# Performance work log

Measured on AMD Instinct MI355X. Metric: run time of the kernel, lower is better.

The kernel has to match this reference:

```python
import jax, jax.numpy as jnp
import numpy as np

D_MODEL = 1024
NHEAD = 16
HEAD_DIM = D_MODEL // NHEAD
SCALE = 1.0 / np.sqrt(HEAD_DIM).astype(np.float32)
B, L = 2, 2048
NEG_INF = -1e30


def setup_inputs() -> dict:
    key = jax.random.key(0)
    ks = jax.random.split(key, 12)
    xav = np.sqrt(6.0 / (D_MODEL + D_MODEL)).astype(np.float32)  # xavier_uniform gain=1
    def lin_w(k):
        return jax.random.uniform(k, (D_MODEL, D_MODEL), jnp.float32, -xav, xav)
    x = jax.random.normal(ks[0], (B, L, D_MODEL), jnp.float32)
    role_mask = jax.random.randint(ks[1], (B, L), 0, 2, jnp.int32)
    # causal attention mask: True = masked (upper triangle above diagonal)
    attn_mask = jnp.triu(jnp.ones((L, L), jnp.bool_), k=1)
    # random key padding: True = padded key
    key_padding_mask = jax.random.randint(ks[2], (B, L), 0, 2, jnp.int32).astype(jnp.bool_)
    return {
        "x": x,
        "role_mask": role_mask,
        "attn_mask": attn_mask,
        "key_padding_mask": key_padding_mask,
        "Wq": lin_w(ks[3]), "bq": jnp.zeros((D_MODEL,), jnp.float32),
        "Wk": lin_w(ks[4]), "bk": jnp.zeros((D_MODEL,), jnp.float32),
        "Wv": lin_w(ks[5]), "bv": jnp.zeros((D_MODEL,), jnp.float32),
        "Wo": lin_w(ks[6]), "bo": jnp.zeros((D_MODEL,), jnp.float32),
        "delta": jnp.asarray(1.0, jnp.float32),
    }


def reference(x, role_mask, attn_mask, key_padding_mask,
              Wq, bq, Wk, bk, Wv, bv, Wo, bo, delta):
    Bb, Ll, Dd = x.shape
    def heads(t):  # [B,L,D] -> [B,H,L,hd]
        return t.reshape(Bb, Ll, NHEAD, HEAD_DIM).transpose(0, 2, 1, 3)
    Q = heads(x @ Wq.T + bq)
    K = heads(x @ Wk.T + bk)
    V = heads(x @ Wv.T + bv)
    scores = jnp.einsum('bhqd,bhkd->bhqk', Q, K) * SCALE  # [B,H,L,L]
    same_role = (role_mask[:, :, None] == role_mask[:, None, :])  # [B,L,L]
    scores = scores + (same_role.astype(scores.dtype) * delta)[:, None, :, :]
    scores = jnp.where(attn_mask[None, None, :, :], -jnp.inf, scores)
    scores = jnp.where(key_padding_mask[:, None, None, :], -jnp.inf, scores)
    attn = jax.nn.softmax(scores, axis=-1)
    attn = jnp.nan_to_num(attn, nan=0.0, posinf=0.0, neginf=0.0)
    out = jnp.einsum('bhqk,bhkd->bhqd', attn, V)
    out = out.transpose(0, 2, 1, 3).reshape(Bb, Ll, Dd)
    return out @ Wo.T + bo
```

## Files before the change

kernel.cpp:

```cpp
#include <hip/hip_runtime.h>
#include <hip/hip_bf16.h>

#define DM 1024
#define NH 16
#define HD 64
#define BB 2
#define LL 2048
#define BL (BB * LL)
#define SCALE 0.125f
#define NEG_BIG -1e30f
#define LOG2E 1.4426950408889634f
#define SC2 (SCALE * LOG2E)
#define FIXM 16.0f
#define SLOTB 8448
#define POOL0_SLOTS 960

typedef __bf16 bf16;
typedef __bf16 bf16x8 __attribute__((ext_vector_type(8)));
typedef __bf16 bf16x4 __attribute__((ext_vector_type(4)));
typedef float f32x4 __attribute__((ext_vector_type(4)));

static __device__ inline bf16x8 load8(const bf16* p) {
    return *reinterpret_cast<const bf16x8*>(p);
}

static __device__ inline float scrub(float x) {
    union { float f; unsigned u; } c; c.f = x;
    return ((c.u & 0x7F800000u) == 0x7F800000u) ? 0.f : x;
}

typedef __attribute__((address_space(1))) const unsigned char ga_t;
typedef __attribute__((address_space(3))) unsigned char ls_t;
static __device__ inline void gload_lds16(const void* g, void* l) {
    __builtin_amdgcn_global_load_lds((ga_t*)g, (ls_t*)l, 16, 0, 0);
}

__global__ __launch_bounds__(256) void prep_all(
    const float* __restrict__ x,
    const float* __restrict__ Wq, const float* __restrict__ Wk,
    const float* __restrict__ Wv, const float* __restrict__ Wo,
    bf16* __restrict__ xb, bf16* __restrict__ Wqb, bf16* __restrict__ Wkb,
    bf16* __restrict__ Wvb, bf16* __restrict__ Wob)
{
    const int tid = threadIdx.x;
    const int gid = blockIdx.x;
    const float* src; bf16* dst; size_t base;
    if (gid < 1024) { src = x; dst = xb; base = (size_t)gid * 1024; }
    else {
        const int wsel = (gid - 1024) >> 8;
        src = (wsel == 0) ? Wq : (wsel == 1) ? Wk : (wsel == 2) ? Wv : Wo;
        dst = (wsel == 0) ? Wqb : (wsel == 1) ? Wkb : (wsel == 2) ? Wvb : Wob;
        base = (size_t)((gid - 1024) & 255) * 1024;
    }
#pragma unroll
    for (int it = 0; it < 4; it++) {
        const size_t i = base + it * 256 + tid;
        const f32x4 v = ((const f32x4*)src)[i];
        bf16x4 o;
        o[0] = (bf16)v[0]; o[1] = (bf16)v[1]; o[2] = (bf16)v[2]; o[3] = (bf16)v[3];
        ((bf16x4*)dst)[i] = o;
    }
}

__global__ __launch_bounds__(256) void compact_meta(
    const int* __restrict__ role, const void* __restrict__ kpad,
    const float* __restrict__ deltap,
    float* __restrict__ biasC, int* __restrict__ cntq, int* __restrict__ cpos,
    bf16* __restrict__ kwc)
{
    const int b = blockIdx.x;
    const int tid = threadIdx.x;
    const unsigned char* kb = (const unsigned char*)kpad;
    int f3F = 0, fLow = 0, fOff = 0;
    for (int i = (tid & 63); i < BL; i += 64) {
        const unsigned char v = kb[i];
        if (v == 0x3F) f3F = 1;
        if ((i & 3) < 2 && v) fLow = 1;
        if ((i & 3) && v) fOff = 1;
    }
    const int mode = __any(f3F) ? (__any(fLow) ? 3 : 2) : (__any(fOff) ? 1 : 0);

    __shared__ int ssum[256];
    int loc[8]; int s = 0;
#pragma unroll
    for (int j = 0; j < 8; j++) {
        const int i = tid * 8 + j, idx = b * LL + i;
        const bool pad = (mode == 0) ? (((const int*)kpad)[idx] != 0)
                       : (mode == 1) ? (((const unsigned char*)kpad)[idx] != 0)
                       : (mode == 2) ? (((const float*)kpad)[idx] != 0.f)
                                     : (((const unsigned short*)kpad)[idx] != 0);
        loc[j] = pad ? 0 : 1; s += loc[j];
    }
    ssum[tid] = s; __syncthreads();
    for (int off = 1; off < 256; off <<= 1) {
        const int t = (tid >= off) ? ssum[tid - off] : 0;
        __syncthreads();
        ssum[tid] += t;
        __syncthreads();
    }
    const int nv = ssum[255];
    int run = ssum[tid] - s;
    const float d2 = scrub(deltap[0]) * LOG2E;
#pragma unroll
    for (int j = 0; j < 8; j++) {
        const int i = tid * 8 + j, idx = b * LL + i;
        const int inc = run + loc[j];
        cntq[idx] = inc;
        if (loc[j]) {
            const int cp = inc - 1;
            const int r = role[idx];
            biasC[b * LL + cp]      = -FIXM + ((r == 0) ? d2 : 0.f);
            biasC[BL + b * LL + cp] = -FIXM + ((r == 1) ? d2 : 0.f);
            cpos[idx] = cp;
        } else cpos[idx] = -1;
        run = inc;
    }
    for (int i = nv + tid; i < LL; i += 256) {
        biasC[b * LL + i] = NEG_BIG;
        biasC[BL + b * LL + i] = NEG_BIG;
    }
    const int roundv = (nv + 63) & ~63;
    const int nt = roundv - nv;
    bf16x8 z;
#pragma unroll
    for (int j = 0; j < 8; j++) z[j] = (bf16)0.f;
    for (int u = tid; u < nt * NH * 8; u += 256) {
        const int c8 = u & 7; const int t2 = u >> 3;
        const int h = t2 / nt; const int rr = nv + t2 % nt;
        *(bf16x8*)&kwc[(((size_t)(b * NH + h) * LL) + rr) * HD + c8 * 8] = z;
    }
}

__global__ __launch_bounds__(256) void qkv_bf16(
    const bf16* __restrict__ xb,
    const bf16* __restrict__ Wqb, const bf16* __restrict__ Wkb, const bf16* __restrict__ Wvb,
    const float* __restrict__ bq, const float* __restrict__ bk, const float* __restrict__ bv,
    bf16* __restrict__ qw, bf16* __restrict__ kwc, bf16* __restrict__ vwc,
    const int* __restrict__ cpos)
{
    __shared__ bf16 As[128 * 32];
    __shared__ bf16 Bs[128 * 32];
    const int tid = threadIdx.x;
    const int lane = tid & 63, w = tid >> 6;
    const int wm = w >> 1, wn = w & 1;
    const int ln = lane & 15, quad = lane >> 4;

    const int lin = blockIdx.y * 32 + blockIdx.x;
    const int xcd = lin & 7;
    const int t = lin >> 3;
    const int mloc = t & 3;
    const int yy = t >> 2;
    const int m0 = (xcd * 4 + mloc) * 128;
    const int sel = yy >> 3;
    const int nloc0 = (yy & 7) * 128;

    const bf16* Wb = (sel == 0) ? Wqb : ((sel == 1) ? Wkb : Wvb);
    const float* bias = (sel == 0) ? bq : ((sel == 1) ? bk : bv);
    bf16* dstw = (sel == 0) ? qw : ((sel == 1) ? kwc : vwc);

    const int rA = lane >> 2;
    const int cA = (lane & 3) * 8;

    f32x4 acc[4][4] = {};
    for (int k0 = 0; k0 < DM; k0 += 32) {
        __syncthreads();
#pragma unroll
        for (int s = 0; s < 2; s++) {
            const int r0 = s * 64 + w * 16;
            gload_lds16(xb + (size_t)(m0 + r0 + rA) * DM + k0 + cA, &As[r0 * 32]);
            gload_lds16(Wb + (size_t)(nloc0 + r0 + rA) * DM + k0 + cA, &Bs[r0 * 32]);
        }
        __syncthreads();
        bf16x8 a[4], b[4];
#pragma unroll
        for (int mi = 0; mi < 4; mi++)
            a[mi] = *(bf16x8*)&As[(wm * 64 + mi * 16 + ln) * 32 + quad * 8];
#pragma unroll
        for (int ni = 0; ni < 4; ni++)
            b[ni] = *(bf16x8*)&Bs[(wn * 64 + ni * 16 + ln) * 32 + quad * 8];
#pragma unroll
        for (int mi = 0; mi < 4; mi++)
#pragma unroll
            for (int ni = 0; ni < 4; ni++)
                acc[mi][ni] = __builtin_amdgcn_mfma_f32_16x16x32_bf16(a[mi], b[ni], acc[mi][ni], 0, 0, 0);
    }

#pragma unroll
    for (int mi = 0; mi < 4; mi++) {
#pragma unroll
        for (int i = 0; i < 4; i++) {
            const int row = m0 + wm * 64 + mi * 16 + quad * 4 + i;
            const int bb = row >> 11, llr = row & (LL - 1);
            const int cp = (sel == 0) ? llr : cpos[bb * LL + llr];
#pragma unroll
            for (int ni = 0; ni < 4; ni++) {
                const int ncol = nloc0 + wn * 64 + ni * 16 + ln;
                const int hh = ncol >> 6, dd = ncol & 63;
                const bf16 v = (bf16)scrub(acc[mi][ni][i] + bias[ncol]);
                if (cp >= 0)
                    dstw[(((size_t)(bb * NH + hh) * LL) + cp) * HD + dd] = v;
            }
        }
    }
}

__global__ __launch_bounds__(256) void vtrans(
    const bf16* __restrict__ vwc, bf16* __restrict__ vtc, const int* __restrict__ cntq)
{
    __shared__ bf16 T[64][72];
    const int l0 = blockIdx.x * 64;
    const int bh = blockIdx.y;
    const int b = bh >> 4;
    const int nv = cntq[b * LL + LL - 1];
    if (l0 >= ((nv + 63) & ~63)) return;
    const int tid = threadIdx.x;
#pragma unroll
    for (int it = 0; it < 2; it++) {
        const int idx = it * 256 + tid;
        const int row = idx >> 3, c8 = (idx & 7) * 8;
        const int wc = (((c8 >> 3) ^ ((row >> 3) & 7))) * 8;
        bf16x8 val;
#pragma unroll
        for (int j = 0; j < 8; j++) val[j] = (bf16)0.f;
        if (l0 + row < nv) val = load8(vwc + ((size_t)bh * LL + l0 + row) * HD + c8);
        *(bf16x8*)&T[row][wc] = val;
    }
    __syncthreads();
#pragma unroll
    for (int it = 0; it < 2; it++) {
        const int idx = it * 256 + tid;
        const int dd = idx >> 3, pg = (idx & 7) * 8;
        bf16x8 o;
#pragma unroll
        for (int j = 0; j < 8; j++) {
            const int r = pg + j;
            o[j] = T[r][(dd & 7) + ((((dd >> 3) ^ ((r >> 3) & 7))) << 3)];
        }
        *(bf16x8*)(vtc + ((size_t)bh * HD + dd) * LL + l0 + pg) = o;
    }
}

__global__ __launch_bounds__(256) void attn_v14(
    const bf16* __restrict__ qw, const bf16* __restrict__ kwc, const bf16* __restrict__ vtc,
    const int* __restrict__ role, const float* __restrict__ biasC, const int* __restrict__ cntq,
    char* __restrict__ pool0, char* __restrict__ pool1,
    bf16* __restrict__ attn_out)
{
    const int lin = blockIdx.y * 60 + blockIdx.x;
    const int xcd = lin & 7;
    const int t = lin >> 3;
    const int xg = t % 60;
    const int g = t / 60;
    const int bh = g * 8 + xcd;

    int qb, c;
    if (xg < 24)      { qb = 31 - xg / 3; c = xg % 3; }
    else if (xg < 48) { qb = 23 - (xg - 24) / 2; c = (xg - 24) % 2; }
    else              { qb = 59 - xg; c = 0; }
    const int nch = (qb + 12) / 12;

    __shared__ bf16 Ks[2][2][64 * 32];
    __shared__ bf16 Vs[2][2][64 * 32];

    const int tid = threadIdx.x;
    const int lane = tid & 63, w = tid >> 6;
    const int col = lane & 15, quad = lane >> 4;
    const int h = bh & (NH - 1), b = bh >> 4;
    const int q0 = qb * 64 + w * 16;

    const bf16* qbase = qw + (size_t)((b * NH + h) * LL) * HD;
    const bf16* kbase = kwc + (size_t)((b * NH + h) * LL) * HD;
    const bf16* vbase = vtc + (size_t)((b * NH + h) * HD) * LL;
    const int* rrow = role + b * LL;

    const int srow = lane >> 2;
    const int sslot = w * 16 + srow;
    const int trueK = ((sslot >> 5) & 1) * 32 + ((sslot >> 2) & 3) * 8
                    + ((sslot >> 4) & 1) * 4 + (sslot & 3);
    const int swz = ((lane & 3) ^ ((lane >> 3) & 3)) * 8;
    const bf16* ksrc = kbase + (size_t)trueK * HD + swz;
    const bf16* vsrc = vbase + (size_t)(w * 16 + srow) * LL + swz;

    bf16x8 qf[2];
    qf[0] = load8(qbase + (size_t)(q0 + col) * HD + quad * 8);
    qf[1] = load8(qbase + (size_t)(q0 + col) * HD + 32 + quad * 8);

    bf16x8 ones;
#pragma unroll
    for (int j = 0; j < 8; j++) ones[j] = (bf16)1.0f;

    const int qabs = q0 + col;
    const int role_q = rrow[qabs];
    const int cnt_q = cntq[b * LL + qabs];
    const float* bp = biasC + (size_t)role_q * BL + b * LL;

    const int cb = cntq[b * LL + qb * 64 + 63];
    const int Tb = (cb + 63) >> 6;
    const int t0c = (c * Tb) / nch;
    const int t1c = ((c + 1) * Tb) / nch;

    f32x4 ol = {};
    f32x4 o[4] = {};

    if (t0c < t1c) {
        const int kp = t0c * 64;
#pragma unroll
        for (int st = 0; st < 2; st++)
            gload_lds16(ksrc + (size_t)kp * HD + st * 32, &Ks[0][st][w * 512]);
#pragma unroll
        for (int kh = 0; kh < 2; kh++)
            gload_lds16(vsrc + kp + kh * 32, &Vs[0][kh][w * 512]);
    }

    const int rs = (quad ^ ((col >> 1) & 3)) * 8;

    for (int kt = t0c; kt < t1c; kt++) {
        const int cur = (kt - t0c) & 1;
        __syncthreads();

        if (kt + 1 < t1c) {
            const int k1 = (kt + 1) * 64;
#pragma unroll
            for (int st = 0; st < 2; st++)
                gload_lds16(ksrc + (size_t)k1 * HD + st * 32, &Ks[cur ^ 1][st][w * 512]);
#pragma unroll
            for (int kh = 0; kh < 2; kh++)
                gload_lds16(vsrc + k1 + kh * 32, &Vs[cur ^ 1][kh][w * 512]);
        }

        const int k0 = kt * 64;

        f32x4 s[4] = {};
#pragma unroll
        for (int st = 0; st < 2; st++) {
#pragma unroll
            for (int ns = 0; ns < 4; ns++) {
                const bf16x8 kf = *(bf16x8*)&Ks[cur][st][(ns * 16 + col) * 32 + rs];
                s[ns] = __builtin_amdgcn_mfma_f32_16x16x32_bf16(kf, qf[st], s[ns], 0, 0, 0);
            }
        }

        bf16x8 pf[2];
#pragma unroll
        for (int ns = 0; ns < 4; ns++) {
            const int kb_ = k0 + ((ns >> 1) << 5) + (quad << 3) + ((ns & 1) << 2);
            const f32x4 bv4 = *(const f32x4*)&bp[kb_];
#pragma unroll
            for (int i = 0; i < 4; i++) {
                float sv = fmaf(s[ns][i], SC2, bv4[i]);
                if ((kb_ + i) >= cnt_q) sv = NEG_BIG;
                pf[ns >> 1][(ns & 1) * 4 + i] = (bf16)exp2f(sv);
            }
        }

#pragma unroll
        for (int ns = 0; ns < 4; ns++) {
#pragma unroll
            for (int kh = 0; kh < 2; kh++) {
                const bf16x8 vf = *(bf16x8*)&Vs[cur][kh][(ns * 16 + col) * 32 + rs];
                o[ns] = __builtin_amdgcn_mfma_f32_16x16x32_bf16(vf, pf[kh], o[ns], 0, 0, 0);
            }
        }
#pragma unroll
        for (int kh = 0; kh < 2; kh++)
            ol = __builtin_amdgcn_mfma_f32_16x16x32_bf16(ones, pf[kh], ol, 0, 0, 0);
    }

    if (nch == 1) {
        const float inv = (ol[0] > 0.f) ? 1.f / ol[0] : 0.f;
        bf16* orow = attn_out + ((size_t)(b * LL) + qabs) * DM + h * HD;
#pragma unroll
        for (int ns = 0; ns < 4; ns++) {
            bf16x4 ov;
#pragma unroll
            for (int i = 0; i < 4; i++) ov[i] = (bf16)scrub(o[ns][i] * inv);
            *(bf16x4*)&orow[ns * 16 + quad * 4] = ov;
        }
    } else {
        const int base = (qb <= 23) ? (qb - 12) * 2 : 24 + (qb - 24) * 3;
        const int slot = bh * 48 + base + c;
        char* ptr = (slot < POOL0_SLOTS) ? (pool0 + (size_t)slot * SLOTB)
                                         : (pool1 + (size_t)(slot - POOL0_SLOTS) * SLOTB);
        bf16* op = (bf16*)ptr;
        float* lp = (float*)(ptr + 8192);
        const int r = w * 16 + col;
        if (quad == 0) lp[r] = ol[0];
#pragma unroll
        for (int ns = 0; ns < 4; ns++) {
            bf16x4 ov;
#pragma unroll
            for (int i = 0; i < 4; i++) ov[i] = (bf16)scrub(o[ns][i]);
            *(bf16x4*)&op[r * 64 + ns * 16 + quad * 4] = ov;
        }
    }
}

__global__ __launch_bounds__(256) void combine(
    const char* __restrict__ pool0, const char* __restrict__ pool1,
    bf16* __restrict__ attn_out)
{
    const int qb = 12 + blockIdx.x;
    const int bh = blockIdx.y;
    const int h = bh & (NH - 1), b = bh >> 4;
    const int nch = (qb + 12) / 12;
    const int base = (qb <= 23) ? (qb - 12) * 2 : 24 + (qb - 24) * 3;

    const char* ptr[3];
    for (int c = 0; c < nch; c++) {
        const int slot = bh * 48 + base + c;
        ptr[c] = (slot < POOL0_SLOTS) ? (pool0 + (size_t)slot * SLOTB)
                                      : (pool1 + (size_t)(slot - POOL0_SLOTS) * SLOTB);
    }

    __shared__ float linv[64];
    const int tid = threadIdx.x;
    if (tid < 64) {
        float ls = 0.f;
        for (int c = 0; c < nch; c++) ls += ((const float*)(ptr[c] + 8192))[tid];
        linv[tid] = (ls > 0.f) ? 1.f / ls : 0.f;
    }
    __syncthreads();

    const int r = tid >> 2;
    const int d0 = (tid & 3) * 16;
    float acc[16] = {};
    for (int c = 0; c < nch; c++) {
        const bf16* op = (const bf16*)ptr[c];
#pragma unroll
        for (int half = 0; half < 2; half++) {
            const bf16x8 v = load8(op + r * 64 + d0 + half * 8);
#pragma unroll
            for (int j = 0; j < 8; j++) acc[half * 8 + j] += (float)v[j];
        }
    }
    const float inv = linv[r];
    bf16x8 outv[2];
#pragma unroll
    for (int half = 0; half < 2; half++)
#pragma unroll
        for (int j = 0; j < 8; j++)
            outv[half][j] = (bf16)scrub(acc[half * 8 + j] * inv);
    bf16* orow = attn_out + ((size_t)(b * LL) + qb * 64 + r) * DM + h * HD + d0;
    *(bf16x8*)orow = outv[0];
    *(bf16x8*)(orow + 8) = outv[1];
}

__global__ __launch_bounds__(256) void out_bf16(
    const bf16* __restrict__ A, const bf16* __restrict__ Wb,
    const float* __restrict__ bias, float* __restrict__ out)
{
    __shared__ bf16 As[128 * 32];
    __shared__ bf16 Bs[64 * 32];
    const int tid = threadIdx.x;
    const int lane = tid & 63, w = tid >> 6;
    const int ln = lane & 15, quad = lane >> 4;

    const int lin = blockIdx.y * 32 + blockIdx.x;
    const int xcd = lin & 7;
    const int t = lin >> 3;
    const int mloc = t & 3;
    const int n = t >> 2;
    const int m0 = (xcd * 4 + mloc) * 128;
    const int n0 = n * 64;

    const int rA = lane >> 2;
    const int cA = (lane & 3) * 8;

    f32x4 acc[2][4] = {};
    for (int k0 = 0; k0 < DM; k0 += 32) {
        __syncthreads();
#pragma unroll
        for (int s = 0; s < 2; s++) {
            const int r0 = s * 64 + w * 16;
            gload_lds16(A + (size_t)(m0 + r0 + rA) * DM + k0 + cA, &As[r0 * 32]);
        }
        gload_lds16(Wb + (size_t)(n0 + w * 16 + rA) * DM + k0 + cA, &Bs[w * 16 * 32]);
        __syncthreads();
        bf16x8 a[2], b[4];
#pragma unroll
        for (int mi = 0; mi < 2; mi++)
            a[mi] = *(bf16x8*)&As[(w * 32 + mi * 16 + ln) * 32 + quad * 8];
#pragma unroll
        for (int ni = 0; ni < 4; ni++)
            b[ni] = *(bf16x8*)&Bs[(ni * 16 + ln) * 32 + quad * 8];
#pragma unroll
        for (int mi = 0; mi < 2; mi++)
#pragma unroll
            for (int ni = 0; ni < 4; ni++)
                acc[mi][ni] = __builtin_amdgcn_mfma_f32_16x16x32_bf16(a[mi], b[ni], acc[mi][ni], 0, 0, 0);
    }
#pragma unroll
    for (int mi = 0; mi < 2; mi++) {
#pragma unroll
        for (int ni = 0; ni < 4; ni++) {
            const int ncol = n0 + ni * 16 + ln;
            const float bv_ = bias[ncol];
#pragma unroll
            for (int i = 0; i < 4; i++) {
                const int row = m0 + w * 32 + mi * 16 + quad * 4 + i;
                out[(size_t)row * DM + ncol] = scrub(acc[mi][ni][i] + bv_);
            }
        }
    }
}

extern "C" void kernel_launch(void* const* d_in, const int* in_sizes, int n_in,
                              void* d_out, int out_size, void* d_ws, size_t ws_size,
                              hipStream_t stream) {
    const float* x    = (const float*)d_in[0];
    const int*   role = (const int*)d_in[1];
    const void*  kpad = d_in[3];
    const float* Wq = (const float*)d_in[4];
    const float* bq = (const float*)d_in[5];
    const float* Wk = (const float*)d_in[6];
    const float* bk = (const float*)d_in[7];
    const float* Wv = (const float*)d_in[8];
    const float* bv = (const float*)d_in[9];
    const float* Wo = (const float*)d_in[10];
    const float* bo = (const float*)d_in[11];
    const float* dl = (const float*)d_in[12];

    char* ws = (char*)d_ws;
    bf16* qw   = (bf16*)(ws);
    bf16* kwc  = (bf16*)(ws + (size_t)(8u  << 20));
    bf16* Wqb  = (bf16*)(ws + (size_t)(16u << 20));
    bf16* Wkb  = (bf16*)(ws + (size_t)(18u << 20));
    bf16* Wvb  = (bf16*)(ws + (size_t)(20u << 20));
    char* pool0 = ws + (size_t)(16u << 20);
    bf16* vwc  = (bf16*)(ws + (size_t)(24u << 20));
    bf16* aw   = (bf16*)(ws + (size_t)(24u << 20));
    bf16* vtc  = (bf16*)(ws + (size_t)(32u << 20));
    bf16* xb   = (bf16*)(ws + (size_t)(40u << 20));
    char* pool1 = ws + (size_t)(40u << 20);
    float* biasC = (float*)(ws + (size_t)(48u << 20));
    int*   cntq  = (int*)(ws + (size_t)(48u << 20) + 32768);
    int*   cpos  = (int*)(ws + (size_t)(48u << 20) + 49152);
    bf16* Wob  = (bf16*)(ws + (size_t)(48u << 20) + 65536);
    float* out = (float*)d_out;

    prep_all<<<dim3(2048), dim3(256), 0, stream>>>(
        x, Wq, Wk, Wv, Wo, xb, Wqb, Wkb, Wvb, Wob);
    compact_meta<<<dim3(2), dim3(256), 0, stream>>>(
        role, kpad, dl, biasC, cntq, cpos, kwc);
    qkv_bf16<<<dim3(32, 24), dim3(256), 0, stream>>>(
        xb, Wqb, Wkb, Wvb, bq, bk, bv, qw, kwc, vwc, cpos);
    vtrans<<<dim3(32, 32), dim3(256), 0, stream>>>(vwc, vtc, cntq);
    attn_v14<<<dim3(60, 32), dim3(256), 0, stream>>>(
        qw, kwc, vtc, role, biasC, cntq, pool0, pool1, aw);
    combine<<<dim3(20, 32), dim3(256), 0, stream>>>(pool0, pool1, aw);
    out_bf16<<<dim3(32, 16), dim3(256), 0, stream>>>(aw, Wob, bo, out);
}
```

Baseline: 218.4 us.

## Fuse meta compaction into prep kernel and widen GEMM K-tiles with XOR swizzle

Merges the compact_meta kernel into prep_all as two extra blocks, removing one kernel launch. The QKV and output-projection GEMMs now stage K-tiles of 64 instead of 32, with XOR-swizzled LDS columns to avoid bank conflicts. This halves the number of barrier pairs per GEMM. The cost is double the LDS footprint per block, which may lower occupancy.

```diff
diff --git a/kernel.cpp b/kernel.cpp
--- a/kernel.cpp
+++ b/kernel.cpp
@@ -40,36 +40,34 @@
     const float* __restrict__ Wq, const float* __restrict__ Wk,
     const float* __restrict__ Wv, const float* __restrict__ Wo,
     bf16* __restrict__ xb, bf16* __restrict__ Wqb, bf16* __restrict__ Wkb,
-    bf16* __restrict__ Wvb, bf16* __restrict__ Wob)
-{
-    const int tid = threadIdx.x;
-    const int gid = blockIdx.x;
-    const float* src; bf16* dst; size_t base;
-    if (gid < 1024) { src = x; dst = xb; base = (size_t)gid * 1024; }
-    else {
-        const int wsel = (gid - 1024) >> 8;
-        src = (wsel == 0) ? Wq : (wsel == 1) ? Wk : (wsel == 2) ? Wv : Wo;
-        dst = (wsel == 0) ? Wqb : (wsel == 1) ? Wkb : (wsel == 2) ? Wvb : Wob;
-        base = (size_t)((gid - 1024) & 255) * 1024;
-    }
-#pragma unroll
-    for (int it = 0; it < 4; it++) {
-        const size_t i = base + it * 256 + tid;
-        const f32x4 v = ((const f32x4*)src)[i];
-        bf16x4 o;
-        o[0] = (bf16)v[0]; o[1] = (bf16)v[1]; o[2] = (bf16)v[2]; o[3] = (bf16)v[3];
-        ((bf16x4*)dst)[i] = o;
-    }
-}
-
-__global__ __launch_bounds__(256) void compact_meta(
+    bf16* __restrict__ Wvb, bf16* __restrict__ Wob,
     const int* __restrict__ role, const void* __restrict__ kpad,
     const float* __restrict__ deltap,
     float* __restrict__ biasC, int* __restrict__ cntq, int* __restrict__ cpos,
     bf16* __restrict__ kwc)
 {
-    const int b = blockIdx.x;
     const int tid = threadIdx.x;
+    const int gid = blockIdx.x;
+    if (gid < 2048) {
+        const float* src; bf16* dst; size_t base;
+        if (gid < 1024) { src = x; dst = xb; base = (size_t)gid * 1024; }
+        else {
+            const int wsel = (gid - 1024) >> 8;
+            src = (wsel == 0) ? Wq : (wsel == 1) ? Wk : (wsel == 2) ? Wv : Wo;
+            dst = (wsel == 0) ? Wqb : (wsel == 1) ? Wkb : (wsel == 2) ? Wvb : Wob;
+            base = (size_t)((gid - 1024) & 255) * 1024;
+        }
+#pragma unroll
+        for (int it = 0; it < 4; it++) {
+            const size_t i = base + it * 256 + tid;
+            const f32x4 v = ((const f32x4*)src)[i];
+            bf16x4 o;
+            o[0] = (bf16)v[0]; o[1] = (bf16)v[1]; o[2] = (bf16)v[2]; o[3] = (bf16)v[3];
+            ((bf16x4*)dst)[i] = o;
+        }
+        return;
+    }
+    const int b = gid - 2048;
     const unsigned char* kb = (const unsigned char*)kpad;
     int f3F = 0, fLow = 0, fOff = 0;
     for (int i = (tid & 63); i < BL; i += 64) {
@@ -138,8 +136,8 @@
     bf16* __restrict__ qw, bf16* __restrict__ kwc, bf16* __restrict__ vwc,
     const int* __restrict__ cpos)
 {
-    __shared__ bf16 As[128 * 32];
-    __shared__ bf16 Bs[128 * 32];
+    __shared__ bf16 As[128 * 64];
+    __shared__ bf16 Bs[128 * 64];
     const int tid = threadIdx.x;
     const int lane = tid & 63, w = tid >> 6;
     const int wm = w >> 1, wn = w & 1;
@@ -158,31 +156,36 @@
     const float* bias = (sel == 0) ? bq : ((sel == 1) ? bk : bv);
     bf16* dstw = (sel == 0) ? qw : ((sel == 1) ? kwc : vwc);
 
-    const int rA = lane >> 2;
-    const int cA = (lane & 3) * 8;
+    const int r8 = lane >> 3;
+    const int swzc = ((lane & 7) ^ r8) * 8;
+    const int lsw = ln & 7;
 
     f32x4 acc[4][4] = {};
-    for (int k0 = 0; k0 < DM; k0 += 32) {
-        __syncthreads();
-#pragma unroll
-        for (int s = 0; s < 2; s++) {
-            const int r0 = s * 64 + w * 16;
-            gload_lds16(xb + (size_t)(m0 + r0 + rA) * DM + k0 + cA, &As[r0 * 32]);
-            gload_lds16(Wb + (size_t)(nloc0 + r0 + rA) * DM + k0 + cA, &Bs[r0 * 32]);
-        }
-        __syncthreads();
-        bf16x8 a[4], b[4];
-#pragma unroll
-        for (int mi = 0; mi < 4; mi++)
-            a[mi] = *(bf16x8*)&As[(wm * 64 + mi * 16 + ln) * 32 + quad * 8];
-#pragma unroll
-        for (int ni = 0; ni < 4; ni++)
-            b[ni] = *(bf16x8*)&Bs[(wn * 64 + ni * 16 + ln) * 32 + quad * 8];
-#pragma unroll
-        for (int mi = 0; mi < 4; mi++)
+    for (int k0 = 0; k0 < DM; k0 += 64) {
+        __syncthreads();
+#pragma unroll
+        for (int s = 0; s < 4; s++) {
+            const int r0 = s * 32 + w * 8;
+            gload_lds16(xb + (size_t)(m0 + r0 + r8) * DM + k0 + swzc, &As[r0 * 64]);
+            gload_lds16(Wb + (size_t)(nloc0 + r0 + r8) * DM + k0 + swzc, &Bs[r0 * 64]);
+        }
+        __syncthreads();
+#pragma unroll
+        for (int kk = 0; kk < 2; kk++) {
+            const int rc = ((kk * 4 + quad) ^ lsw) * 8;
+            bf16x8 a[4], b[4];
+#pragma unroll
+            for (int mi = 0; mi < 4; mi++)
+                a[mi] = *(bf16x8*)&As[(wm * 64 + mi * 16 + ln) * 64 + rc];
 #pragma unroll
             for (int ni = 0; ni < 4; ni++)
-                acc[mi][ni] = __builtin_amdgcn_mfma_f32_16x16x32_bf16(a[mi], b[ni], acc[mi][ni], 0, 0, 0);
+                b[ni] = *(bf16x8*)&Bs[(wn * 64 + ni * 16 + ln) * 64 + rc];
+#pragma unroll
+            for (int mi = 0; mi < 4; mi++)
+#pragma unroll
+                for (int ni = 0; ni < 4; ni++)
+                    acc[mi][ni] = __builtin_amdgcn_mfma_f32_16x16x32_bf16(a[mi], b[ni], acc[mi][ni], 0, 0, 0);
+        }
     }
 
 #pragma unroll
@@ -449,8 +452,8 @@
     const bf16* __restrict__ A, const bf16* __restrict__ Wb,
     const float* __restrict__ bias, float* __restrict__ out)
 {
-    __shared__ bf16 As[128 * 32];
-    __shared__ bf16 Bs[64 * 32];
+    __shared__ bf16 As[128 * 64];
+    __shared__ bf16 Bs[64 * 64];
     const int tid = threadIdx.x;
     const int lane = tid & 63, w = tid >> 6;
     const int ln = lane & 15, quad = lane >> 4;
@@ -463,31 +466,40 @@
     const int m0 = (xcd * 4 + mloc) * 128;
     const int n0 = n * 64;
 
-    const int rA = lane >> 2;
-    const int cA = (lane & 3) * 8;
+    const int r8 = lane >> 3;
+    const int swzc = ((lane & 7) ^ r8) * 8;
+    const int lsw = ln & 7;
 
     f32x4 acc[2][4] = {};
-    for (int k0 = 0; k0 < DM; k0 += 32) {
-        __syncthreads();
+    for (int k0 = 0; k0 < DM; k0 += 64) {
+        __syncthreads();
+#pragma unroll
+        for (int s = 0; s < 4; s++) {
+            const int r0 = s * 32 + w * 8;
+            gload_lds16(A + (size_t)(m0 + r0 + r8) * DM + k0 + swzc, &As[r0 * 64]);
+        }
 #pragma unroll
         for (int s = 0; s < 2; s++) {
-            const int r0 = s * 64 + w * 16;
-            gload_lds16(A + (size_t)(m0 + r0 + rA) * DM + k0 + cA, &As[r0 * 32]);
-        }
-        gload_lds16(Wb + (size_t)(n0 + w * 16 + rA) * DM + k0 + cA, &Bs[w * 16 * 32]);
-        __syncthreads();
-        bf16x8 a[2], b[4];
-#pragma unroll
-        for (int mi = 0; mi < 2; mi++)
-            a[mi] = *(bf16x8*)&As[(w * 32 + mi * 16 + ln) * 32 + quad * 8];
-#pragma unroll
-        for (int ni = 0; ni < 4; ni++)
-            b[ni] = *(bf16x8*)&Bs[(ni * 16 + ln) * 32 + quad * 8];
-#pragma unroll
-        for (int mi = 0; mi < 2; mi++)
+            const int r0 = s * 32 + w * 8;
+            gload_lds16(Wb + (size_t)(n0 + r0 + r8) * DM + k0 + swzc, &Bs[r0 * 64]);
+        }
+        __syncthreads();
+#pragma unroll
+        for (int kk = 0; kk < 2; kk++) {
+            const int rc = ((kk * 4 + quad) ^ lsw) * 8;
+            bf16x8 a[2], b[4];
+#pragma unroll
+            for (int mi = 0; mi < 2; mi++)
+                a[mi] = *(bf16x8*)&As[(w * 32 + mi * 16 + ln) * 64 + rc];
 #pragma unroll
             for (int ni = 0; ni < 4; ni++)
-                acc[mi][ni] = __builtin_amdgcn_mfma_f32_16x16x32_bf16(a[mi], b[ni], acc[mi][ni], 0, 0, 0);
+                b[ni] = *(bf16x8*)&Bs[(ni * 16 + ln) * 64 + rc];
+#pragma unroll
+            for (int mi = 0; mi < 2; mi++)
+#pragma unroll
+                for (int ni = 0; ni < 4; ni++)
+                    acc[mi][ni] = __builtin_amdgcn_mfma_f32_16x16x32_bf16(a[mi], b[ni], acc[mi][ni], 0, 0, 0);
+        }
     }
 #pragma unroll
     for (int mi = 0; mi < 2; mi++) {
@@ -538,9 +550,8 @@
     bf16* Wob  = (bf16*)(ws + (size_t)(48u << 20) + 65536);
     float* out = (float*)d_out;
 
-    prep_all<<<dim3(2048), dim3(256), 0, stream>>>(
-        x, Wq, Wk, Wv, Wo, xb, Wqb, Wkb, Wvb, Wob);
-    compact_meta<<<dim3(2), dim3(256), 0, stream>>>(
+    prep_all<<<dim3(2050), dim3(256), 0, stream>>>(
+        x, Wq, Wk, Wv, Wo, xb, Wqb, Wkb, Wvb, Wob,
         role, kpad, dl, biasC, cntq, cpos, kwc);
     qkv_bf16<<<dim3(32, 24), dim3(256), 0, stream>>>(
         xb, Wqb, Wkb, Wvb, bq, bk, bv, qw, kwc, vwc, cpos);
```

Result: slower. 224.9 us (+3.0%).

## Double-buffer LDS in projection GEMMs and merge metadata prep into conversion kernel

Applied to the files above, without the earlier changes.

The QKV and output projection GEMMs now use two LDS buffers. The next K-tile's global-to-LDS loads are issued before the current tile's MFMAs, which halves the barriers per iteration and overlaps memory latency with compute. The small compact_meta kernel is folded into prep_all as two extra blocks, removing a kernel launch. LDS usage doubles per block, which may reduce occupancy.

```diff
diff --git a/kernel.cpp b/kernel.cpp
--- a/kernel.cpp
+++ b/kernel.cpp
@@ -40,36 +40,34 @@
     const float* __restrict__ Wq, const float* __restrict__ Wk,
     const float* __restrict__ Wv, const float* __restrict__ Wo,
     bf16* __restrict__ xb, bf16* __restrict__ Wqb, bf16* __restrict__ Wkb,
-    bf16* __restrict__ Wvb, bf16* __restrict__ Wob)
-{
-    const int tid = threadIdx.x;
-    const int gid = blockIdx.x;
-    const float* src; bf16* dst; size_t base;
-    if (gid < 1024) { src = x; dst = xb; base = (size_t)gid * 1024; }
-    else {
-        const int wsel = (gid - 1024) >> 8;
-        src = (wsel == 0) ? Wq : (wsel == 1) ? Wk : (wsel == 2) ? Wv : Wo;
-        dst = (wsel == 0) ? Wqb : (wsel == 1) ? Wkb : (wsel == 2) ? Wvb : Wob;
-        base = (size_t)((gid - 1024) & 255) * 1024;
-    }
-#pragma unroll
-    for (int it = 0; it < 4; it++) {
-        const size_t i = base + it * 256 + tid;
-        const f32x4 v = ((const f32x4*)src)[i];
-        bf16x4 o;
-        o[0] = (bf16)v[0]; o[1] = (bf16)v[1]; o[2] = (bf16)v[2]; o[3] = (bf16)v[3];
-        ((bf16x4*)dst)[i] = o;
-    }
-}
-
-__global__ __launch_bounds__(256) void compact_meta(
+    bf16* __restrict__ Wvb, bf16* __restrict__ Wob,
     const int* __restrict__ role, const void* __restrict__ kpad,
     const float* __restrict__ deltap,
     float* __restrict__ biasC, int* __restrict__ cntq, int* __restrict__ cpos,
     bf16* __restrict__ kwc)
 {
-    const int b = blockIdx.x;
     const int tid = threadIdx.x;
+    const int gid = blockIdx.x;
+    if (gid < 2048) {
+        const float* src; bf16* dst; size_t base;
+        if (gid < 1024) { src = x; dst = xb; base = (size_t)gid * 1024; }
+        else {
+            const int wsel = (gid - 1024) >> 8;
+            src = (wsel == 0) ? Wq : (wsel == 1) ? Wk : (wsel == 2) ? Wv : Wo;
+            dst = (wsel == 0) ? Wqb : (wsel == 1) ? Wkb : (wsel == 2) ? Wvb : Wob;
+            base = (size_t)((gid - 1024) & 255) * 1024;
+        }
+#pragma unroll
+        for (int it = 0; it < 4; it++) {
+            const size_t i = base + it * 256 + tid;
+            const f32x4 v = ((const f32x4*)src)[i];
+            bf16x4 o;
+            o[0] = (bf16)v[0]; o[1] = (bf16)v[1]; o[2] = (bf16)v[2]; o[3] = (bf16)v[3];
+            ((bf16x4*)dst)[i] = o;
+        }
+        return;
+    }
+    const int b = gid - 2048;
     const unsigned char* kb = (const unsigned char*)kpad;
     int f3F = 0, fLow = 0, fOff = 0;
     for (int i = (tid & 63); i < BL; i += 64) {
@@ -138,8 +136,8 @@
     bf16* __restrict__ qw, bf16* __restrict__ kwc, bf16* __restrict__ vwc,
     const int* __restrict__ cpos)
 {
-    __shared__ bf16 As[128 * 32];
-    __shared__ bf16 Bs[128 * 32];
+    __shared__ bf16 As[2][128 * 32];
+    __shared__ bf16 Bs[2][128 * 32];
     const int tid = threadIdx.x;
     const int lane = tid & 63, w = tid >> 6;
     const int wm = w >> 1, wn = w & 1;
@@ -160,29 +158,42 @@
 
     const int rA = lane >> 2;
     const int cA = (lane & 3) * 8;
+    const bf16* asrc = xb + (size_t)(m0 + rA) * DM + cA;
+    const bf16* bsrc = Wb + (size_t)(nloc0 + rA) * DM + cA;
+
+#pragma unroll
+    for (int s = 0; s < 2; s++) {
+        const int r0 = s * 64 + w * 16;
+        gload_lds16(asrc + (size_t)r0 * DM, &As[0][r0 * 32]);
+        gload_lds16(bsrc + (size_t)r0 * DM, &Bs[0][r0 * 32]);
+    }
+    __syncthreads();
 
     f32x4 acc[4][4] = {};
+    int cur = 0;
     for (int k0 = 0; k0 < DM; k0 += 32) {
-        __syncthreads();
-#pragma unroll
-        for (int s = 0; s < 2; s++) {
-            const int r0 = s * 64 + w * 16;
-            gload_lds16(xb + (size_t)(m0 + r0 + rA) * DM + k0 + cA, &As[r0 * 32]);
-            gload_lds16(Wb + (size_t)(nloc0 + r0 + rA) * DM + k0 + cA, &Bs[r0 * 32]);
-        }
-        __syncthreads();
+        if (k0 + 32 < DM) {
+#pragma unroll
+            for (int s = 0; s < 2; s++) {
+                const int r0 = s * 64 + w * 16;
+                gload_lds16(asrc + (size_t)r0 * DM + k0 + 32, &As[cur ^ 1][r0 * 32]);
+                gload_lds16(bsrc + (size_t)r0 * DM + k0 + 32, &Bs[cur ^ 1][r0 * 32]);
+            }
+        }
         bf16x8 a[4], b[4];
 #pragma unroll
         for (int mi = 0; mi < 4; mi++)
-            a[mi] = *(bf16x8*)&As[(wm * 64 + mi * 16 + ln) * 32 + quad * 8];
+            a[mi] = *(bf16x8*)&As[cur][(wm * 64 + mi * 16 + ln) * 32 + quad * 8];
 #pragma unroll
         for (int ni = 0; ni < 4; ni++)
-            b[ni] = *(bf16x8*)&Bs[(wn * 64 + ni * 16 + ln) * 32 + quad * 8];
+            b[ni] = *(bf16x8*)&Bs[cur][(wn * 64 + ni * 16 + ln) * 32 + quad * 8];
 #pragma unroll
         for (int mi = 0; mi < 4; mi++)
 #pragma unroll
             for (int ni = 0; ni < 4; ni++)
                 acc[mi][ni] = __builtin_amdgcn_mfma_f32_16x16x32_bf16(a[mi], b[ni], acc[mi][ni], 0, 0, 0);
+        __syncthreads();
+        cur ^= 1;
     }
 
 #pragma unroll
@@ -449,8 +460,8 @@
     const bf16* __restrict__ A, const bf16* __restrict__ Wb,
     const float* __restrict__ bias, float* __restrict__ out)
 {
-    __shared__ bf16 As[128 * 32];
-    __shared__ bf16 Bs[64 * 32];
+    __shared__ bf16 As[2][128 * 32];
+    __shared__ bf16 Bs[2][64 * 32];
     const int tid = threadIdx.x;
     const int lane = tid & 63, w = tid >> 6;
     const int ln = lane & 15, quad = lane >> 4;
@@ -465,29 +476,42 @@
 
     const int rA = lane >> 2;
     const int cA = (lane & 3) * 8;
+    const bf16* asrc = A + (size_t)(m0 + rA) * DM + cA;
+    const bf16* bsrc = Wb + (size_t)(n0 + rA) * DM + cA;
+
+#pragma unroll
+    for (int s = 0; s < 2; s++) {
+        const int r0 = s * 64 + w * 16;
+        gload_lds16(asrc + (size_t)r0 * DM, &As[0][r0 * 32]);
+    }
+    gload_lds16(bsrc + (size_t)(w * 16) * DM, &Bs[0][w * 16 * 32]);
+    __syncthreads();
 
     f32x4 acc[2][4] = {};
+    int cur = 0;
     for (int k0 = 0; k0 < DM; k0 += 32) {
-        __syncthreads();
-#pragma unroll
-        for (int s = 0; s < 2; s++) {
-            const int r0 = s * 64 + w * 16;
-            gload_lds16(A + (size_t)(m0 + r0 + rA) * DM + k0 + cA, &As[r0 * 32]);
-        }
-        gload_lds16(Wb + (size_t)(n0 + w * 16 + rA) * DM + k0 + cA, &Bs[w * 16 * 32]);
-        __syncthreads();
+        if (k0 + 32 < DM) {
+#pragma unroll
+            for (int s = 0; s < 2; s++) {
+                const int r0 = s * 64 + w * 16;
+                gload_lds16(asrc + (size_t)r0 * DM + k0 + 32, &As[cur ^ 1][r0 * 32]);
+            }
+            gload_lds16(bsrc + (size_t)(w * 16) * DM + k0 + 32, &Bs[cur ^ 1][w * 16 * 32]);
+        }
         bf16x8 a[2], b[4];
 #pragma unroll
         for (int mi = 0; mi < 2; mi++)
-            a[mi] = *(bf16x8*)&As[(w * 32 + mi * 16 + ln) * 32 + quad * 8];
+            a[mi] = *(bf16x8*)&As[cur][(w * 32 + mi * 16 + ln) * 32 + quad * 8];
 #pragma unroll
         for (int ni = 0; ni < 4; ni++)
-            b[ni] = *(bf16x8*)&Bs[(ni * 16 + ln) * 32 + quad * 8];
+            b[ni] = *(bf16x8*)&Bs[cur][(ni * 16 + ln) * 32 + quad * 8];
 #pragma unroll
         for (int mi = 0; mi < 2; mi++)
 #pragma unroll
             for (int ni = 0; ni < 4; ni++)
                 acc[mi][ni] = __builtin_amdgcn_mfma_f32_16x16x32_bf16(a[mi], b[ni], acc[mi][ni], 0, 0, 0);
+        __syncthreads();
+        cur ^= 1;
     }
 #pragma unroll
     for (int mi = 0; mi < 2; mi++) {
@@ -538,9 +562,8 @@
     bf16* Wob  = (bf16*)(ws + (size_t)(48u << 20) + 65536);
     float* out = (float*)d_out;
 
-    prep_all<<<dim3(2048), dim3(256), 0, stream>>>(
-        x, Wq, Wk, Wv, Wo, xb, Wqb, Wkb, Wvb, Wob);
-    compact_meta<<<dim3(2), dim3(256), 0, stream>>>(
+    prep_all<<<dim3(2050), dim3(256), 0, stream>>>(
+        x, Wq, Wk, Wv, Wo, xb, Wqb, Wkb, Wvb, Wob,
         role, kpad, dl, biasC, cntq, cpos, kwc);
     qkv_bf16<<<dim3(32, 24), dim3(256), 0, stream>>>(
         xb, Wqb, Wkb, Wvb, bq, bk, bv, qw, kwc, vwc, cpos);
```

New measurement: 223.8 us. 1.02x slower.

## Fuse metadata compaction into prep kernel and gather-compact K/V projection rows

Applied to the files above, without the earlier changes.

Merges the compact_meta kernel into prep_all as two extra blocks, removing one kernel launch. The metadata pass now writes an inverse index (compact position to source row) instead of a forward scatter index. The K/V projection blocks gather only the non-padded input rows through that index and exit early for tiles beyond the valid count, so roughly half of the K/V GEMM work (padded keys) is skipped. Risks: the gathered A-tile loads are less contiguous, and correctness depends on the padding count being read before the tiles run.

```diff
diff --git a/kernel.cpp b/kernel.cpp
--- a/kernel.cpp
+++ b/kernel.cpp
@@ -40,36 +40,34 @@
     const float* __restrict__ Wq, const float* __restrict__ Wk,
     const float* __restrict__ Wv, const float* __restrict__ Wo,
     bf16* __restrict__ xb, bf16* __restrict__ Wqb, bf16* __restrict__ Wkb,
-    bf16* __restrict__ Wvb, bf16* __restrict__ Wob)
+    bf16* __restrict__ Wvb, bf16* __restrict__ Wob,
+    const int* __restrict__ role, const void* __restrict__ kpad,
+    const float* __restrict__ deltap,
+    float* __restrict__ biasC, int* __restrict__ cntq, int* __restrict__ ipos,
+    bf16* __restrict__ kwc)
 {
     const int tid = threadIdx.x;
     const int gid = blockIdx.x;
-    const float* src; bf16* dst; size_t base;
-    if (gid < 1024) { src = x; dst = xb; base = (size_t)gid * 1024; }
-    else {
-        const int wsel = (gid - 1024) >> 8;
-        src = (wsel == 0) ? Wq : (wsel == 1) ? Wk : (wsel == 2) ? Wv : Wo;
-        dst = (wsel == 0) ? Wqb : (wsel == 1) ? Wkb : (wsel == 2) ? Wvb : Wob;
-        base = (size_t)((gid - 1024) & 255) * 1024;
-    }
-#pragma unroll
-    for (int it = 0; it < 4; it++) {
-        const size_t i = base + it * 256 + tid;
-        const f32x4 v = ((const f32x4*)src)[i];
-        bf16x4 o;
-        o[0] = (bf16)v[0]; o[1] = (bf16)v[1]; o[2] = (bf16)v[2]; o[3] = (bf16)v[3];
-        ((bf16x4*)dst)[i] = o;
-    }
-}
-
-__global__ __launch_bounds__(256) void compact_meta(
-    const int* __restrict__ role, const void* __restrict__ kpad,
-    const float* __restrict__ deltap,
-    float* __restrict__ biasC, int* __restrict__ cntq, int* __restrict__ cpos,
-    bf16* __restrict__ kwc)
-{
-    const int b = blockIdx.x;
-    const int tid = threadIdx.x;
+    if (gid < 2048) {
+        const float* src; bf16* dst; size_t base;
+        if (gid < 1024) { src = x; dst = xb; base = (size_t)gid * 1024; }
+        else {
+            const int wsel = (gid - 1024) >> 8;
+            src = (wsel == 0) ? Wq : (wsel == 1) ? Wk : (wsel == 2) ? Wv : Wo;
+            dst = (wsel == 0) ? Wqb : (wsel == 1) ? Wkb : (wsel == 2) ? Wvb : Wob;
+            base = (size_t)((gid - 1024) & 255) * 1024;
+        }
+#pragma unroll
+        for (int it = 0; it < 4; it++) {
+            const size_t i = base + it * 256 + tid;
+            const f32x4 v = ((const f32x4*)src)[i];
+            bf16x4 o;
+            o[0] = (bf16)v[0]; o[1] = (bf16)v[1]; o[2] = (bf16)v[2]; o[3] = (bf16)v[3];
+            ((bf16x4*)dst)[i] = o;
+        }
+        return;
+    }
+    const int b = gid - 2048;
     const unsigned char* kb = (const unsigned char*)kpad;
     int f3F = 0, fLow = 0, fOff = 0;
     for (int i = (tid & 63); i < BL; i += 64) {
@@ -111,8 +109,8 @@
             const int r = role[idx];
             biasC[b * LL + cp]      = -FIXM + ((r == 0) ? d2 : 0.f);
             biasC[BL + b * LL + cp] = -FIXM + ((r == 1) ? d2 : 0.f);
-            cpos[idx] = cp;
-        } else cpos[idx] = -1;
+            ipos[b * LL + cp] = i;
+        }
         run = inc;
     }
     for (int i = nv + tid; i < LL; i += 256) {
@@ -136,7 +134,7 @@
     const bf16* __restrict__ Wqb, const bf16* __restrict__ Wkb, const bf16* __restrict__ Wvb,
     const float* __restrict__ bq, const float* __restrict__ bk, const float* __restrict__ bv,
     bf16* __restrict__ qw, bf16* __restrict__ kwc, bf16* __restrict__ vwc,
-    const int* __restrict__ cpos)
+    const int* __restrict__ ipos, const int* __restrict__ cntq)
 {
     __shared__ bf16 As[128 * 32];
     __shared__ bf16 Bs[128 * 32];
@@ -150,9 +148,19 @@
     const int t = lin >> 3;
     const int mloc = t & 3;
     const int yy = t >> 2;
-    const int m0 = (xcd * 4 + mloc) * 128;
+    const int mt = xcd * 4 + mloc;
     const int sel = yy >> 3;
     const int nloc0 = (yy & 7) * 128;
+
+    int b = 0, cp0 = 0, nvb = 0, m0 = 0;
+    if (sel == 0) {
+        m0 = mt * 128;
+    } else {
+        b = mt >> 4;
+        cp0 = (mt & 15) * 128;
+        nvb = cntq[b * LL + LL - 1];
+        if (cp0 >= nvb) return;
+    }
 
     const bf16* Wb = (sel == 0) ? Wqb : ((sel == 1) ? Wkb : Wvb);
     const float* bias = (sel == 0) ? bq : ((sel == 1) ? bk : bv);
@@ -161,44 +169,63 @@
     const int rA = lane >> 2;
     const int cA = (lane & 3) * 8;
 
+    const bf16* asrc[2];
+#pragma unroll
+    for (int s = 0; s < 2; s++) {
+        const int r = s * 64 + w * 16 + rA;
+        int grow;
+        if (sel == 0) grow = m0 + r;
+        else {
+            const int cp = cp0 + r;
+            grow = b * LL + ((cp < nvb) ? ipos[b * LL + cp] : 0);
+        }
+        asrc[s] = xb + (size_t)grow * DM + cA;
+    }
+
     f32x4 acc[4][4] = {};
     for (int k0 = 0; k0 < DM; k0 += 32) {
         __syncthreads();
 #pragma unroll
         for (int s = 0; s < 2; s++) {
             const int r0 = s * 64 + w * 16;
-            gload_lds16(xb + (size_t)(m0 + r0 + rA) * DM + k0 + cA, &As[r0 * 32]);
+            gload_lds16(asrc[s] + k0, &As[r0 * 32]);
             gload_lds16(Wb + (size_t)(nloc0 + r0 + rA) * DM + k0 + cA, &Bs[r0 * 32]);
         }
         __syncthreads();
-        bf16x8 a[4], b[4];
+        bf16x8 a[4], bfr[4];
 #pragma unroll
         for (int mi = 0; mi < 4; mi++)
             a[mi] = *(bf16x8*)&As[(wm * 64 + mi * 16 + ln) * 32 + quad * 8];
 #pragma unroll
         for (int ni = 0; ni < 4; ni++)
-            b[ni] = *(bf16x8*)&Bs[(wn * 64 + ni * 16 + ln) * 32 + quad * 8];
+            bfr[ni] = *(bf16x8*)&Bs[(wn * 64 + ni * 16 + ln) * 32 + quad * 8];
 #pragma unroll
         for (int mi = 0; mi < 4; mi++)
 #pragma unroll
             for (int ni = 0; ni < 4; ni++)
-                acc[mi][ni] = __builtin_amdgcn_mfma_f32_16x16x32_bf16(a[mi], b[ni], acc[mi][ni], 0, 0, 0);
+                acc[mi][ni] = __builtin_amdgcn_mfma_f32_16x16x32_bf16(a[mi], bfr[ni], acc[mi][ni], 0, 0, 0);
     }
 
 #pragma unroll
     for (int mi = 0; mi < 4; mi++) {
 #pragma unroll
         for (int i = 0; i < 4; i++) {
-            const int row = m0 + wm * 64 + mi * 16 + quad * 4 + i;
-            const int bb = row >> 11, llr = row & (LL - 1);
-            const int cp = (sel == 0) ? llr : cpos[bb * LL + llr];
+            const int rr = wm * 64 + mi * 16 + quad * 4 + i;
+            int batch, drow; bool valid;
+            if (sel == 0) {
+                const int row = m0 + rr;
+                batch = row >> 11; drow = row & (LL - 1); valid = true;
+            } else {
+                const int cp = cp0 + rr;
+                batch = b; drow = cp; valid = (cp < nvb);
+            }
 #pragma unroll
             for (int ni = 0; ni < 4; ni++) {
                 const int ncol = nloc0 + wn * 64 + ni * 16 + ln;
                 const int hh = ncol >> 6, dd = ncol & 63;
                 const bf16 v = (bf16)scrub(acc[mi][ni][i] + bias[ncol]);
-                if (cp >= 0)
-                    dstw[(((size_t)(bb * NH + hh) * LL) + cp) * HD + dd] = v;
+                if (valid)
+                    dstw[(((size_t)(batch * NH + hh) * LL) + drow) * HD + dd] = v;
             }
         }
     }
@@ -534,16 +561,15 @@
     char* pool1 = ws + (size_t)(40u << 20);
     float* biasC = (float*)(ws + (size_t)(48u << 20));
     int*   cntq  = (int*)(ws + (size_t)(48u << 20) + 32768);
-    int*   cpos  = (int*)(ws + (size_t)(48u << 20) + 49152);
+    int*   ipos  = (int*)(ws + (size_t)(48u << 20) + 49152);
     bf16* Wob  = (bf16*)(ws + (size_t)(48u << 20) + 65536);
     float* out = (float*)d_out;
 
-    prep_all<<<dim3(2048), dim3(256), 0, stream>>>(
-        x, Wq, Wk, Wv, Wo, xb, Wqb, Wkb, Wvb, Wob);
-    compact_meta<<<dim3(2), dim3(256), 0, stream>>>(
-        role, kpad, dl, biasC, cntq, cpos, kwc);
+    prep_all<<<dim3(2050), dim3(256), 0, stream>>>(
+        x, Wq, Wk, Wv, Wo, xb, Wqb, Wkb, Wvb, Wob,
+        role, kpad, dl, biasC, cntq, ipos, kwc);
     qkv_bf16<<<dim3(32, 24), dim3(256), 0, stream>>>(
-        xb, Wqb, Wkb, Wvb, bq, bk, bv, qw, kwc, vwc, cpos);
+        xb, Wqb, Wkb, Wvb, bq, bk, bv, qw, kwc, vwc, ipos, cntq);
     vtrans<<<dim3(32, 32), dim3(256), 0, stream>>>(vwc, vtc, cntq);
     attn_v14<<<dim3(60, 32), dim3(256), 0, stream>>>(
         qw, kwc, vtc, role, biasC, cntq, pool0, pool1, aw);
```

New measurement: 220.1 us (median of 2 runs). About the same (+0.8%).
